# Performance work log

Hardware: AMD Instinct MI355X
Metric: run time of the kernel (lower is better)

## Reference

```python
import jax, jax.numpy as jnp
import numpy as np

B, S, D, H, DH = 4, 1024, 1024, 16, 64  # batch, seq, d_model, heads, head dim (d_Q=d_K=d_V)


def setup_inputs() -> dict:
    key = jax.random.key(0)
    ks = jax.random.split(key, 12)
    std = 0.02
    return {
        "x_Q": jax.random.normal(ks[0], (B, S, D), jnp.float32),
        "x_K": jax.random.normal(ks[1], (B, S, D), jnp.float32),
        "x_V": jax.random.normal(ks[2], (B, S, D), jnp.float32),
        "src_batch_lens": jax.random.randint(ks[3], (B,), 0, S),
        # stacked per-head projection weights: [H, d_model, head_dim]
        "Wq": jax.random.normal(ks[4], (H, D, DH), jnp.float32) * std,
        "bq": jax.random.normal(ks[5], (H, DH), jnp.float32) * std,
        "Wk": jax.random.normal(ks[6], (H, D, DH), jnp.float32) * std,
        "bk": jax.random.normal(ks[7], (H, DH), jnp.float32) * std,
        "Wv": jax.random.normal(ks[8], (H, D, DH), jnp.float32) * std,
        "bv": jax.random.normal(ks[9], (H, DH), jnp.float32) * std,
        "Wo": jax.random.normal(ks[10], (D, D), jnp.float32) * std,
        "bo": jax.random.normal(ks[11], (D,), jnp.float32) * std,
    }


def reference(x_Q, x_K, x_V, src_batch_lens, Wq, bq, Wk, bk, Wv, bv, Wo, bo):
    dq = Wq.shape[-1]
    seq = x_Q.shape[1]
    # all heads at once instead of the per-head python loop
    Q = jnp.einsum('bsd,hde->bhse', x_Q, Wq) + bq[None, :, None, :]
    K = jnp.einsum('bsd,hde->bhse', x_K, Wk) + bk[None, :, None, :]
    V = jnp.einsum('bsd,hde->bhse', x_V, Wv) + bv[None, :, None, :]
    scores = jnp.einsum('bhse,bhte->bhst', Q, K) / jnp.sqrt(jnp.asarray(dq, x_Q.dtype))
    # original: matmul(diag(1..1,0..0), scores) zeroes query rows >= length
    rowmask = (jnp.arange(seq)[None, :] < src_batch_lens[:, None])  # [B, S]
    scores = scores * rowmask[:, None, :, None].astype(scores.dtype)
    A = jax.nn.softmax(scores, axis=-1)  # torch Softmax(dim=2) on [B,S,S] per head = key axis
    AV = jnp.einsum('bhst,bhtv->bhsv', A, V)
    out = AV.transpose(0, 2, 1, 3).reshape(x_Q.shape[0], seq, -1)  # concat heads on dim 2
    return out @ Wo + bo  # dropout p=0 -> identity
```

## Files before the change

### kernel.cpp

```cpp
#include <hip/hip_runtime.h>
#include <stdint.h>

typedef short v8s __attribute__((ext_vector_type(8)));
typedef short v4s __attribute__((ext_vector_type(4)));
typedef float v4f __attribute__((ext_vector_type(4)));

#define AS1 __attribute__((address_space(1)))
#define AS3 __attribute__((address_space(3)))

__device__ __forceinline__ void glds16(const void* g, void* l) {
  __builtin_amdgcn_global_load_lds((const AS1 void*)g, (AS3 void*)l, 16, 0, 0);
}

__device__ __forceinline__ short f2bf(float f) {
  uint32_t u = __float_as_uint(f);
  u += 0x7fffu + ((u >> 16) & 1u);
  return (short)(u >> 16);
}

__global__ __launch_bounds__(256) void prep_kernel(
    const float* __restrict__ xQ, const float* __restrict__ xK, const float* __restrict__ xV,
    const float* __restrict__ wq, const float* __restrict__ wk, const float* __restrict__ wv,
    const float* __restrict__ wo,
    short* __restrict__ oxQ, short* __restrict__ oxK, short* __restrict__ oxV,
    short* __restrict__ oq, short* __restrict__ ok, short* __restrict__ ov,
    short* __restrict__ oo) {
  const int bid = blockIdx.x;
  const int t = threadIdx.x;
  if (bid >= 1024) {
    const int c = bid - 1024;
    const int z = c >> 12;
    const int i = (c & 4095) * 256 + t;
    const float* in = (z == 0) ? xQ : (z == 1) ? xK : xV;
    short* out      = (z == 0) ? oxQ : (z == 1) ? oxK : oxV;
    float4 v = ((const float4*)in)[i];
    short4 o = { f2bf(v.x), f2bf(v.y), f2bf(v.z), f2bf(v.w) };
    ((short4*)out)[i] = o;
    return;
  }
  __shared__ float tile[64][65];
  const float* in;
  short* out;
  int C, R, rb, cb;
  if (bid < 768) {
    const int which = bid >> 8, rem = bid & 255;
    const int slice = rem >> 4, rbi = rem & 15;
    in  = ((which == 0) ? wq : (which == 1) ? wk : wv) + (size_t)slice * 65536;
    out = ((which == 0) ? oq : (which == 1) ? ok : ov) + (size_t)slice * 65536;
    C = 64; R = 1024; rb = rbi * 64; cb = 0;
  } else {
    const int r = bid - 768;
    in = wo; out = oo;
    C = 1024; R = 1024; rb = (r >> 4) * 64; cb = (r & 15) * 64;
  }
  const int col = t & 63, r0 = t >> 6;
#pragma unroll
  for (int i = 0; i < 16; ++i) {
    int row = r0 + i * 4;
    tile[row][col] = in[(size_t)(rb + row) * C + cb + col];
  }
  __syncthreads();
#pragma unroll
  for (int i = 0; i < 16; ++i) {
    int orow = r0 + i * 4;
    out[(size_t)(cb + orow) * R + rb + col] = f2bf(tile[col][orow]);
  }
}

template <int MR>
__device__ __forceinline__ void gemm_core(const short* __restrict__ Ag,
                                          const short* __restrict__ Bg,
                                          short* As, short* Bs,
                                          v4f (&acc)[MR / 32][4]) {
  constexpr int MT = MR / 32;
  constexpr int ASZ = MR * 32;
  constexpr int BSZ = 128 * 32;
  const int tid  = threadIdx.x;
  const int lane = tid & 63;
  const int w    = tid >> 6;
  const int quad = lane >> 4;
  const int c15  = lane & 15;
  const int wr   = (w >> 1) * (MR / 2);
  const int wc   = (w & 1) * 64;

  const int r0 = tid >> 2;
  const int p0 = (tid & 3) ^ ((r0 & 3) ^ ((r0 >> 2) & 3));
  const short* a0 = Ag + (size_t)r0 * 1024 + p0 * 8;
  const short* a1 = a0 + 64 * 1024;
  const short* b0 = Bg + (size_t)r0 * 1024 + p0 * 8;
  const short* b1 = b0 + 64 * 1024;
  short* lA = As + tid * 8;
  short* lB = Bs + tid * 8;

  auto issue = [&](int t, int buf) {
    const int o = t * 32;
    glds16(a0 + o, lA + buf * ASZ);
    if constexpr (MR == 128) glds16(a1 + o, lA + buf * ASZ + 2048);
    glds16(b0 + o, lB + buf * BSZ);
    glds16(b1 + o, lB + buf * BSZ + 2048);
  };

  issue(0, 0);
  issue(1, 1);

  const int xs = (c15 & 3) ^ ((c15 >> 2) & 3);
  const int rdoff = ((quad ^ xs)) * 8;

  for (int kb = 0; kb < 32; ++kb) {
    if constexpr (MR == 128)
      asm volatile("s_waitcnt vmcnt(4)\n\ts_barrier" ::: "memory");
    else
      asm volatile("s_waitcnt vmcnt(3)\n\ts_barrier" ::: "memory");

    const int t2 = kb + 2;
    issue(t2 < 32 ? t2 : 31, t2 % 3);

    const short* Ab = As + (kb % 3) * ASZ;
    const short* Bb = Bs + (kb % 3) * BSZ;

    v8s a[MT], b[4];
#pragma unroll
    for (int mt = 0; mt < MT; ++mt)
      a[mt] = *(const v8s*)(Ab + (wr + mt * 16 + c15) * 32 + rdoff);
#pragma unroll
    for (int nt = 0; nt < 4; ++nt)
      b[nt] = *(const v8s*)(Bb + (wc + nt * 16 + c15) * 32 + rdoff);
#pragma unroll
    for (int mt = 0; mt < MT; ++mt)
#pragma unroll
      for (int nt = 0; nt < 4; ++nt)
        acc[mt][nt] = __builtin_amdgcn_mfma_f32_16x16x32_bf16(a[mt], b[nt], acc[mt][nt], 0, 0, 0);
  }
}

__global__ __launch_bounds__(256, 3) void proj_gemm(
    const short* __restrict__ xQ, const short* __restrict__ xK, const short* __restrict__ xV,
    const short* __restrict__ WqT, const short* __restrict__ WkT, const short* __restrict__ WvT,
    const float* __restrict__ bq, const float* __restrict__ bk, const float* __restrict__ bv,
    short* __restrict__ Qb, short* __restrict__ Kb, short* __restrict__ Vtb) {
  __shared__ short As[12288];
  __shared__ short Bs[12288];
  const int lin = blockIdx.x;
  const int z = lin >> 8;
  const int r = lin & 255;
  const int nb = ((r >> 3) & 7) * 128;
  const int mb = (((r & 7) << 2) + (r >> 6)) * 128;
  const short* A    = (z == 0) ? xQ  : (z == 1) ? xK  : xV;
  const short* Bt   = (z == 0) ? WqT : (z == 1) ? WkT : WvT;
  const float* bias = (z == 0) ? bq  : (z == 1) ? bk  : bv;
  short* outp       = (z == 0) ? Qb  : (z == 1) ? Kb  : Vtb;
  v4f acc[4][4] = {};
  gemm_core<128>(A + (size_t)mb * 1024, Bt + (size_t)nb * 1024, As, Bs, acc);

  const int lane = threadIdx.x & 63, w = threadIdx.x >> 6;
  const int quad = lane >> 4, c15 = lane & 15;
  const int wr = (w >> 1) * 64, wc = (w & 1) * 64;
  const bool vmode = (z == 2);
#pragma unroll
  for (int nt = 0; nt < 4; ++nt) {
    const int gn = nb + wc + nt * 16 + c15;
    const float bb = bias[gn];
    const int h = gn >> 6, e = gn & 63;
#pragma unroll
    for (int mt = 0; mt < 4; ++mt) {
      if (!vmode) {
#pragma unroll
        for (int rr = 0; rr < 4; ++rr) {
          const int gm = mb + wr + mt * 16 + quad * 4 + rr;
          const int bi = gm >> 10, s = gm & 1023;
          const size_t base = (size_t)(bi * 16 + h) * 65536;
          outp[base + (size_t)s * 64 + e] = f2bf(acc[mt][nt][rr] + bb);
        }
      } else {
        const int gm0 = mb + wr + mt * 16 + quad * 4;
        const int bi = gm0 >> 10, s0 = gm0 & 1023;
        const size_t base = (size_t)(bi * 16 + h) * 65536;
        short4 st = { f2bf(acc[mt][nt][0] + bb), f2bf(acc[mt][nt][1] + bb),
                      f2bf(acc[mt][nt][2] + bb), f2bf(acc[mt][nt][3] + bb) };
        *(short4*)&outp[base + (size_t)e * 1024 + s0] = st;
      }
    }
  }
}

__global__ __launch_bounds__(256, 3) void out_gemm(
    const short* __restrict__ AV, const short* __restrict__ WoT,
    const float* __restrict__ bo, float* __restrict__ outp) {
  __shared__ short As[6144];
  __shared__ short Bs[12288];
  const int lin = blockIdx.x;
  const int nb = ((lin >> 3) & 7) * 128;
  const int mb = (((lin & 7) << 3) + (lin >> 6)) * 64;
  v4f acc[2][4] = {};
  gemm_core<64>(AV + (size_t)mb * 1024, WoT + (size_t)nb * 1024, As, Bs, acc);
  const int lane = threadIdx.x & 63, w = threadIdx.x >> 6;
  const int quad = lane >> 4, c15 = lane & 15;
  const int wr = (w >> 1) * 32, wc = (w & 1) * 64;
#pragma unroll
  for (int nt = 0; nt < 4; ++nt) {
    const int gn = nb + wc + nt * 16 + c15;
    const float bb = bo[gn];
#pragma unroll
    for (int mt = 0; mt < 2; ++mt)
#pragma unroll
      for (int r = 0; r < 4; ++r) {
        const int gm = mb + wr + mt * 16 + quad * 4 + r;
        outp[(size_t)gm * 1024 + gn] = acc[mt][nt][r] + bb;
      }
  }
}

__global__ __launch_bounds__(256, 2) void attn_kernel(
    const short* __restrict__ Qb, const short* __restrict__ Kb,
    const short* __restrict__ Vtb, const int* __restrict__ lens,
    short* __restrict__ AVb) {
  __shared__ short Ks[3][4096];
  __shared__ short Vs[3][4096];
  const int tid = threadIdx.x, lane = tid & 63, w = tid >> 6;
  const int quad = lane >> 4, c15 = lane & 15;
  const int flat = blockIdx.x;
  const int bh = (flat & 7) + 8 * ((flat >> 3) & 7);
  const int qg = flat >> 6;
  const int b = bh >> 4, h = bh & 15;
  const short* Qp = Qb  + (size_t)bh * 65536;
  const short* Kp = Kb  + (size_t)bh * 65536;
  const short* Vp = Vtb + (size_t)bh * 65536;
  const int len = lens[b];
  const int row0 = qg * 128 + w * 32;

  v8s bq_[2][2];
#pragma unroll
  for (int qf = 0; qf < 2; ++qf)
#pragma unroll
    for (int kf = 0; kf < 2; ++kf)
      bq_[qf][kf] = *(const v8s*)(Qp + (size_t)(row0 + qf * 16 + c15) * 64 + kf * 32 + quad * 8);

  float scale[2];
  scale[0] = (row0 + c15 < len) ? 0.125f : 0.0f;
  scale[1] = (row0 + 16 + c15 < len) ? 0.125f : 0.0f;
  float sm[2] = {0.f, 0.f};
  v4f o[2][4] = {};

  const int srow = tid >> 3, spart = tid & 7;
  const int gpart = spart ^ (srow & 7);
  const int kgo0 = srow * 64 + gpart * 8, kgo1 = (srow + 32) * 64 + gpart * 8;
  const int vgo0 = srow * 1024 + gpart * 8, vgo1 = (srow + 32) * 1024 + gpart * 8;
  const int l0 = tid * 8, l1 = 2048 + tid * 8;

  const int c7 = c15 & 7;
  const int krow = c15 * 128;
  const int koff0 = krow + ((quad) ^ c7) * 16;
  const int koff1 = krow + ((4 + quad) ^ c7) * 16;
  const int q2 = quad >> 1, h8 = (quad & 1) * 8;
  int voff[4];
#pragma unroll
  for (int nt = 0; nt < 4; ++nt)
    voff[nt] = krow + ((2 * nt + q2) ^ c7) * 16 + h8;

  auto issue = [&](int t) {
    const short* kt = Kp + (size_t)t * 4096;
    const short* vt = Vp + t * 64;
    char* kd = (char*)Ks[t % 3];
    char* vd = (char*)Vs[t % 3];
    glds16(kt + kgo0, kd + l0 * 2);
    glds16(kt + kgo1, kd + l1 * 2);
    glds16(vt + vgo0, vd + l0 * 2);
    glds16(vt + vgo1, vd + l1 * 2);
  };

  auto compute = [&](int kb) {
    const char* kc = (const char*)Ks[kb % 3];
    const char* vc = (const char*)Vs[kb % 3];
    v8s ak[4][2];
#pragma unroll
    for (int nt = 0; nt < 4; ++nt) {
      ak[nt][0] = *(const v8s*)(kc + nt * 2048 + koff0);
      ak[nt][1] = *(const v8s*)(kc + nt * 2048 + koff1);
    }
    v4f sc[2][4];
#pragma unroll
    for (int qf = 0; qf < 2; ++qf)
#pragma unroll
      for (int nt = 0; nt < 4; ++nt) {
        v4f z = {};
#pragma unroll
        for (int kf = 0; kf < 2; ++kf)
          z = __builtin_amdgcn_mfma_f32_16x16x32_bf16(ak[nt][kf], bq_[qf][kf], z, 0, 0, 0);
        sc[qf][nt] = z;
      }
    v4s pb[2][4];
#pragma unroll
    for (int qf = 0; qf < 2; ++qf)
#pragma unroll
      for (int nt = 0; nt < 4; ++nt) {
        v4s pv;
#pragma unroll
        for (int r = 0; r < 4; ++r) {
          float p = __expf(sc[qf][nt][r] * scale[qf]);
          sm[qf] += p;
          pv[r] = f2bf(p);
        }
        pb[qf][nt] = pv;
      }
    v4s av[4][4];
#pragma unroll
    for (int t = 0; t < 4; ++t)
#pragma unroll
      for (int nt = 0; nt < 4; ++nt)
        av[t][nt] = *(const v4s*)(vc + t * 2048 + voff[nt]);
#pragma unroll
    for (int t = 0; t < 4; ++t)
#pragma unroll
      for (int nt = 0; nt < 4; ++nt) {
        o[0][t] = __builtin_amdgcn_mfma_f32_16x16x16bf16_1k(av[t][nt], pb[0][nt], o[0][t], 0, 0, 0);
        o[1][t] = __builtin_amdgcn_mfma_f32_16x16x16bf16_1k(av[t][nt], pb[1][nt], o[1][t], 0, 0, 0);
      }
  };

  issue(0);
  issue(1);

  for (int kb = 0; kb < 15; ++kb) {
    asm volatile("s_waitcnt vmcnt(4)\n\ts_barrier" ::: "memory");
    if (kb <= 13) issue(kb + 2);
    compute(kb);
  }
  asm volatile("s_waitcnt vmcnt(0)\n\ts_barrier" ::: "memory");
  compute(15);

#pragma unroll
  for (int qf = 0; qf < 2; ++qf) {
    float s = sm[qf];
    s += __shfl_xor(s, 16);
    s += __shfl_xor(s, 32);
    const float inv = 1.0f / s;
    const size_t rowbase = (size_t)(b * 1024 + row0 + qf * 16 + c15) * 1024 + h * 64;
#pragma unroll
    for (int t = 0; t < 4; ++t) {
      short4 st = { f2bf(o[qf][t][0] * inv), f2bf(o[qf][t][1] * inv),
                    f2bf(o[qf][t][2] * inv), f2bf(o[qf][t][3] * inv) };
      *(short4*)&AVb[rowbase + t * 16 + quad * 4] = st;
    }
  }
}

extern "C" void kernel_launch(void* const* d_in, const int* in_sizes, int n_in,
                              void* d_out, int out_size, void* d_ws, size_t ws_size,
                              hipStream_t stream) {
  const float* xQ = (const float*)d_in[0];
  const float* xK = (const float*)d_in[1];
  const float* xV = (const float*)d_in[2];
  const int* lens = (const int*)d_in[3];
  const float* Wq = (const float*)d_in[4];
  const float* bq = (const float*)d_in[5];
  const float* Wk = (const float*)d_in[6];
  const float* bk = (const float*)d_in[7];
  const float* Wv = (const float*)d_in[8];
  const float* bv = (const float*)d_in[9];
  const float* Wo = (const float*)d_in[10];
  const float* bo = (const float*)d_in[11];
  float* out = (float*)d_out;

  char* ws = (char*)d_ws;
  short* xQb = (short*)(ws + 0);
  short* xKb = (short*)(ws + 8388608);
  short* xVb = (short*)(ws + 16777216);
  short* WqT = (short*)(ws + 25165824);
  short* WkT = (short*)(ws + 27262976);
  short* WvT = (short*)(ws + 29360128);
  short* WoT = (short*)(ws + 31457280);
  short* Qb  = (short*)(ws + 33554432);
  short* Kb  = (short*)(ws + 41943040);
  short* Vtb = (short*)(ws + 50331648);
  short* AVb = (short*)(ws + 58720256);

  prep_kernel<<<dim3(13312), 256, 0, stream>>>(xQ, xK, xV, Wq, Wk, Wv, Wo,
                                               xQb, xKb, xVb, WqT, WkT, WvT, WoT);
  proj_gemm<<<dim3(768), 256, 0, stream>>>(xQb, xKb, xVb, WqT, WkT, WvT,
                                           bq, bk, bv, Qb, Kb, Vtb);
  attn_kernel<<<dim3(512), 256, 0, stream>>>(Qb, Kb, Vtb, lens, AVb);
  out_gemm<<<dim3(512), 256, 0, stream>>>(AVb, WoT, bo, out);
}
```

Baseline: 203.5 us.

## Fuse fp32-to-bf16 activation conversion into projection GEMM A-tile loading

The prep kernel no longer converts x_Q/x_K/x_V to bf16 in a separate pass. The projection GEMM now loads fp32 activations into registers, converts them with packed bf16 conversion instructions, and writes them into swizzled LDS. It keeps a 3-buffer pipeline with async direct-to-LDS loads for the weights. This removes a full write and re-read of the 24 MB of converted activations, but it doubles the global bytes read for A inside the GEMM and adds register pressure and conversion work to the main loop.

Result: slower. 213.2 us (+4.8%).

```diff
diff --git a/kernel.cpp b/kernel.cpp
--- a/kernel.cpp
+++ b/kernel.cpp
@@ -4,6 +4,7 @@
 typedef short v8s __attribute__((ext_vector_type(8)));
 typedef short v4s __attribute__((ext_vector_type(4)));
 typedef float v4f __attribute__((ext_vector_type(4)));
+typedef uint32_t v2u __attribute__((ext_vector_type(2)));
 
 #define AS1 __attribute__((address_space(1)))
 #define AS3 __attribute__((address_space(3)))
@@ -18,26 +19,21 @@
   return (short)(u >> 16);
 }
 
+__device__ __forceinline__ uint32_t cvtpk(float lo, float hi) {
+  uint32_t r;
+  asm("v_cvt_pk_bf16_f32 %0, %1, %2" : "=v"(r) : "v"(lo), "v"(hi));
+  return r;
+}
+
+#define MFMA16(A, B, C) __builtin_amdgcn_mfma_f32_16x16x32_bf16(A, B, C, 0, 0, 0)
+
 __global__ __launch_bounds__(256) void prep_kernel(
-    const float* __restrict__ xQ, const float* __restrict__ xK, const float* __restrict__ xV,
     const float* __restrict__ wq, const float* __restrict__ wk, const float* __restrict__ wv,
     const float* __restrict__ wo,
-    short* __restrict__ oxQ, short* __restrict__ oxK, short* __restrict__ oxV,
     short* __restrict__ oq, short* __restrict__ ok, short* __restrict__ ov,
     short* __restrict__ oo) {
   const int bid = blockIdx.x;
   const int t = threadIdx.x;
-  if (bid >= 1024) {
-    const int c = bid - 1024;
-    const int z = c >> 12;
-    const int i = (c & 4095) * 256 + t;
-    const float* in = (z == 0) ? xQ : (z == 1) ? xK : xV;
-    short* out      = (z == 0) ? oxQ : (z == 1) ? oxK : oxV;
-    float4 v = ((const float4*)in)[i];
-    short4 o = { f2bf(v.x), f2bf(v.y), f2bf(v.z), f2bf(v.w) };
-    ((short4*)out)[i] = o;
-    return;
-  }
   __shared__ float tile[64][65];
   const float* in;
   short* out;
@@ -134,7 +130,7 @@
 }
 
 __global__ __launch_bounds__(256, 3) void proj_gemm(
-    const short* __restrict__ xQ, const short* __restrict__ xK, const short* __restrict__ xV,
+    const float* __restrict__ xQ, const float* __restrict__ xK, const float* __restrict__ xV,
     const short* __restrict__ WqT, const short* __restrict__ WkT, const short* __restrict__ WvT,
     const float* __restrict__ bq, const float* __restrict__ bk, const float* __restrict__ bv,
     short* __restrict__ Qb, short* __restrict__ Kb, short* __restrict__ Vtb) {
@@ -145,16 +141,99 @@
   const int r = lin & 255;
   const int nb = ((r >> 3) & 7) * 128;
   const int mb = (((r & 7) << 2) + (r >> 6)) * 128;
-  const short* A    = (z == 0) ? xQ  : (z == 1) ? xK  : xV;
+  const float* Af   = (z == 0) ? xQ  : (z == 1) ? xK  : xV;
   const short* Bt   = (z == 0) ? WqT : (z == 1) ? WkT : WvT;
   const float* bias = (z == 0) ? bq  : (z == 1) ? bk  : bv;
   short* outp       = (z == 0) ? Qb  : (z == 1) ? Kb  : Vtb;
-  v4f acc[4][4] = {};
-  gemm_core<128>(A + (size_t)mb * 1024, Bt + (size_t)nb * 1024, As, Bs, acc);
-
-  const int lane = threadIdx.x & 63, w = threadIdx.x >> 6;
+
+  const int tid = threadIdx.x, lane = tid & 63, w = tid >> 6;
   const int quad = lane >> 4, c15 = lane & 15;
   const int wr = (w >> 1) * 64, wc = (w & 1) * 64;
+
+  const int r0 = tid >> 2;
+  const int p0 = (tid & 3) ^ ((r0 & 3) ^ ((r0 >> 2) & 3));
+  const short* b0 = Bt + (size_t)(nb + r0) * 1024 + p0 * 8;
+  const short* b1 = b0 + 64 * 1024;
+  short* lB = Bs + tid * 8;
+  auto issueB = [&](int t, int buf) {
+    const int o = t * 32;
+    glds16(b0 + o, lB + buf * 4096);
+    glds16(b1 + o, lB + buf * 4096 + 2048);
+  };
+
+  const int ra = tid >> 3, pa = tid & 7;
+  const float* a0 = Af + (size_t)(mb + ra) * 1024 + pa * 4;
+  const int sR = (ra & 3) ^ ((ra >> 2) & 3);
+  const int adst = ra * 32 + (((pa >> 1) ^ sR) * 8) + (pa & 1) * 4;
+
+  v4f aE[4], aO[4];
+  auto loadA = [&](v4f (&dst)[4], int t) {
+    const float* s = a0 + t * 32;
+    dst[0] = *(const v4f*)(s);
+    dst[1] = *(const v4f*)(s + 32768);
+    dst[2] = *(const v4f*)(s + 65536);
+    dst[3] = *(const v4f*)(s + 98304);
+  };
+  auto writeA = [&](v4f (&src)[4], int buf) {
+    short* d = As + buf * 4096 + adst;
+#pragma unroll
+    for (int j = 0; j < 4; ++j) {
+      v2u pk;
+      pk[0] = cvtpk(src[j][0], src[j][1]);
+      pk[1] = cvtpk(src[j][2], src[j][3]);
+      *(v2u*)(d + j * 1024) = pk;
+    }
+  };
+
+  const int xs = (c15 & 3) ^ ((c15 >> 2) & 3);
+  const int rdoff = (quad ^ xs) * 8;
+  v4f acc[4][4] = {};
+
+  auto compute = [&](int kb) {
+    const short* Ab = As + (kb % 3) * 4096;
+    const short* Bb = Bs + (kb % 3) * 4096;
+    v8s a[4], b[4];
+#pragma unroll
+    for (int mt = 0; mt < 4; ++mt)
+      a[mt] = *(const v8s*)(Ab + (wr + mt * 16 + c15) * 32 + rdoff);
+#pragma unroll
+    for (int nt = 0; nt < 4; ++nt)
+      b[nt] = *(const v8s*)(Bb + (wc + nt * 16 + c15) * 32 + rdoff);
+#pragma unroll
+    for (int mt = 0; mt < 4; ++mt)
+#pragma unroll
+      for (int nt = 0; nt < 4; ++nt)
+        acc[mt][nt] = MFMA16(a[mt], b[nt], acc[mt][nt]);
+  };
+
+  loadA(aE, 0); issueB(0, 0);
+  loadA(aO, 1); issueB(1, 1);
+  writeA(aE, 0);
+  asm volatile("s_waitcnt lgkmcnt(0)\n\ts_barrier" ::: "memory");
+
+  for (int p = 0; p < 16; ++p) {
+    {
+      const int R = 2 * p;
+      const int t2 = R + 2, tc = t2 < 32 ? t2 : 31;
+      loadA(aE, tc);
+      issueB(tc, t2 % 3);
+      asm volatile("s_waitcnt vmcnt(8)" ::: "memory");
+      writeA(aO, (R + 1) % 3);
+      compute(R);
+      asm volatile("s_waitcnt lgkmcnt(0)\n\ts_barrier" ::: "memory");
+    }
+    {
+      const int R = 2 * p + 1;
+      const int t2 = R + 2, tc = t2 < 32 ? t2 : 31;
+      loadA(aO, tc);
+      issueB(tc, t2 % 3);
+      asm volatile("s_waitcnt vmcnt(8)" ::: "memory");
+      writeA(aE, (R + 1) % 3);
+      compute(R);
+      asm volatile("s_waitcnt lgkmcnt(0)\n\ts_barrier" ::: "memory");
+    }
+  }
+
   const bool vmode = (z == 2);
 #pragma unroll
   for (int nt = 0; nt < 4; ++nt) {
@@ -362,9 +441,6 @@
   float* out = (float*)d_out;
 
   char* ws = (char*)d_ws;
-  short* xQb = (short*)(ws + 0);
-  short* xKb = (short*)(ws + 8388608);
-  short* xVb = (short*)(ws + 16777216);
   short* WqT = (short*)(ws + 25165824);
   short* WkT = (short*)(ws + 27262976);
   short* WvT = (short*)(ws + 29360128);
@@ -374,9 +450,8 @@
   short* Vtb = (short*)(ws + 50331648);
   short* AVb = (short*)(ws + 58720256);
 
-  prep_kernel<<<dim3(13312), 256, 0, stream>>>(xQ, xK, xV, Wq, Wk, Wv, Wo,
-                                               xQb, xKb, xVb, WqT, WkT, WvT, WoT);
-  proj_gemm<<<dim3(768), 256, 0, stream>>>(xQb, xKb, xVb, WqT, WkT, WvT,
+  prep_kernel<<<dim3(1024), 256, 0, stream>>>(Wq, Wk, Wv, Wo, WqT, WkT, WvT, WoT);
+  proj_gemm<<<dim3(768), 256, 0, stream>>>(xQ, xK, xV, WqT, WkT, WvT,
                                            bq, bk, bv, Qb, Kb, Vtb);
   attn_kernel<<<dim3(512), 256, 0, stream>>>(Qb, Kb, Vtb, lens, AVb);
   out_gemm<<<dim3(512), 256, 0, stream>>>(AVb, WoT, bo, out);
```
